# Optimization experiments

Measured on AMD Instinct MI355X. Metric: run time of the kernel, lower is better.

Reference implementation:

```python
import jax, jax.numpy as jnp
import numpy as np

T, B, H = 2048, 64, 256   # time, batch, hidden/input/memory size
A = 256                   # attention_size
IN = H + H                # cell input size = input_size + memory_size = 512
NEG = -1e12


def setup_inputs() -> dict:
    key = jax.random.key(0)
    ks = jax.random.split(key, 12)
    s = lambda k, shape, fan: jax.random.normal(k, shape, jnp.float32) / np.sqrt(fan)
    inp = {
        "input": jax.random.normal(ks[0], (B, H), jnp.float32),
        "memory": jax.random.normal(ks[1], (T, B, H), jnp.float32),
        "memory_mask": jax.random.bernoulli(ks[2], 0.9, (T, B)),
        "state": jax.random.normal(ks[3], (B, H), jnp.float32),
        # attention MLP: Linear(input+state+memory -> A, no bias), Tanh, Linear(A -> 1, no bias)
        "W_a1": s(ks[4], (H + H + H, A), H * 3),
        "w_a2": s(ks[5], (A,), A),
        # gate: Linear(IN -> IN, no bias) + sigmoid
        "W_gate": s(ks[6], (IN, IN), IN),
        # GRUCell params (torch layout: [3H, in], gates order r,z,n)
        "W_ih": s(ks[7], (3 * H, IN), IN),
        "W_hh": s(ks[8], (3 * H, H), H),
        "b_ih": jnp.zeros((3 * H,), jnp.float32),
        "b_hh": jnp.zeros((3 * H,), jnp.float32),
    }
    return inp


def reference(input, memory, memory_mask, state, W_a1, w_a2, W_gate, W_ih, W_hh, b_ih, b_hh):
    # --- additive attention: tanh(W1 @ [input, state, memory]) @ w2 ---
    # split W_a1 by the concat layout [input | state | memory]
    qs = jnp.concatenate([input, state], axis=-1) @ W_a1[: 2 * H]      # [B, A]
    mp = jnp.einsum("tbh,ha->tba", memory, W_a1[2 * H :])               # [T, B, A]
    logits = jnp.tanh(qs[None] + mp) @ w_a2                              # [T, B]
    logits = jnp.where(memory_mask, logits, NEG)
    scores = jax.nn.softmax(logits, axis=0)                              # [T, B]
    attn_vec = jnp.einsum("tb,tbh->bh", scores, memory)                  # [B, H]

    # --- gate ---
    new_input = jnp.concatenate([input, attn_vec], axis=-1)              # [B, 2H]
    gated = new_input * jax.nn.sigmoid(new_input @ W_gate)

    # --- GRU cell (torch semantics, gates r, z, n) ---
    gi = gated @ W_ih.T + b_ih                                           # [B, 3H]
    gh = state @ W_hh.T + b_hh                                           # [B, 3H]
    i_r, i_z, i_n = jnp.split(gi, 3, axis=-1)
    h_r, h_z, h_n = jnp.split(gh, 3, axis=-1)
    r = jax.nn.sigmoid(i_r + h_r)
    z = jax.nn.sigmoid(i_z + h_z)
    n = jnp.tanh(i_n + r * h_n)
    return (1.0 - z) * n + z * state                                     # [B, H]
```

## Files before the change

kernel.cpp:

```cpp
#include <hip/hip_runtime.h>
#include <hip/hip_bf16.h>

#define B_DIM 64
#define H_DIM 256
#define NCHG 8
#define CHUNKS 4
#define TCH 64

typedef __attribute__((ext_vector_type(8))) short short8;
typedef __attribute__((ext_vector_type(4))) float f32x4;

__device__ __forceinline__ unsigned short bfbits(float f) {
    __hip_bfloat16 h = __float2bfloat16(f);
    unsigned short u;
    __builtin_memcpy(&u, &h, 2);
    return u;
}
__device__ __forceinline__ float fexp(float x) {
    float r;
    asm("v_exp_f32 %0, %1" : "=v"(r) : "v"(x * 1.4426950408889634f));
    return r;
}
__device__ __forceinline__ float ftanh(float x) {
    float e, r;
    asm("v_exp_f32 %0, %1" : "=v"(e) : "v"(x * 2.8853900817779268f));
    asm("v_rcp_f32 %0, %1" : "=v"(r) : "v"(e + 1.0f));
    return 1.0f - 2.0f * r;
}
__device__ __forceinline__ float fast_sigmoid(float x) {
    return 1.0f / (1.0f + __expf(-x));
}

__global__ void prep_qs_kernel(const float* __restrict__ W_a1,
                               const float* __restrict__ input,
                               const float* __restrict__ state,
                               unsigned short* __restrict__ WmT,
                               float* __restrict__ qs) {
    __shared__ float cat[512];
    int bid = blockIdx.x, tid = threadIdx.x;
    if (bid < 256) {
        WmT[tid * 256 + bid] = bfbits(W_a1[(512 + bid) * 256 + tid]);
    } else {
        int b = bid - 256;
        cat[tid] = input[b * 256 + tid];
        cat[256 + tid] = state[b * 256 + tid];
        __syncthreads();
        int a = tid;
        float s0 = 0.f, s1 = 0.f, s2 = 0.f, s3 = 0.f;
        #pragma unroll 4
        for (int k = 0; k < 512; k += 4) {
            s0 += cat[k]     * W_a1[(k)     * 256 + a];
            s1 += cat[k + 1] * W_a1[(k + 1) * 256 + a];
            s2 += cat[k + 2] * W_a1[(k + 2) * 256 + a];
            s3 += cat[k + 3] * W_a1[(k + 3) * 256 + a];
        }
        qs[b * 256 + a] = (s0 + s1) + (s2 + s3);
    }
}

__global__ __launch_bounds__(512, 2) void attn_kernel(
    const float* __restrict__ memory, const int* __restrict__ mask,
    const unsigned short* __restrict__ WmT,
    const float* __restrict__ qs, const float* __restrict__ w_a2,
    float* __restrict__ part_l, float* __restrict__ part_acc)
{
    extern __shared__ char smem[];
    unsigned short* slab0 = (unsigned short*)smem;
    unsigned short* slab1 = (unsigned short*)(smem + 32768);
    float* lpart = (float*)(smem + 65536);
    int*   maskL = (int*)(smem + 65536 + 2048);

    int b = blockIdx.x, g = blockIdx.y;
    int tid = threadIdx.x;
    int lane = tid & 63, w = tid >> 6;
    int lr = lane & 15, lh = lane >> 4;
    int tbase = g * (CHUNKS * TCH);
    const float* mbase = memory + (size_t)tbase * (B_DIM * H_DIM) + b * H_DIM;

    float4 ld[8];
    #pragma unroll
    for (int i = 0; i < 8; ++i)
        ld[i] = *((const float4*)(mbase + (size_t)(i * 8 + w) * (B_DIM * H_DIM)) + lane);

    int wa0 = w * 32;
    short8 areg[8][2];
    #pragma unroll
    for (int kk = 0; kk < 8; ++kk)
        #pragma unroll
        for (int mf = 0; mf < 2; ++mf)
            areg[kk][mf] = *(const short8*)(WmT + (wa0 + mf * 16 + lr) * 256 + kk * 32 + lh * 8);

    float qv[2][4], wv[2][4];
    #pragma unroll
    for (int mf = 0; mf < 2; ++mf)
        #pragma unroll
        for (int r = 0; r < 4; ++r) {
            int a = wa0 + mf * 16 + lh * 4 + r;
            qv[mf][r] = qs[b * 256 + a];
            wv[mf][r] = w_a2[a];
        }

    if (tid < CHUNKS * TCH) maskL[tid] = mask[(tbase + tid) * B_DIM + b];

    int wby = (lane * 8) ^ (w << 4);
    #pragma unroll
    for (int i = 0; i < 8; ++i) {
        ushort4 o;
        o.x = bfbits(ld[i].x); o.y = bfbits(ld[i].y);
        o.z = bfbits(ld[i].z); o.w = bfbits(ld[i].w);
        *(ushort4*)((char*)slab0 + (i * 8 + w) * 512 + wby) = o;
    }
    __syncthreads();

    float a8[8] = {0.f, 0.f, 0.f, 0.f, 0.f, 0.f, 0.f, 0.f};
    float l_acc = 0.f;
    int slice4 = ((lane >> 5) + 2 * w) * 4;
    int hpvb = (lane & 31) * 16;

    for (int s = 0; s < CHUNKS; ++s) {
        const char* cur = (const char*)((s & 1) ? slab1 : slab0);
        char* nxt = (char*)((s & 1) ? slab0 : slab1);

        if (s < CHUNKS - 1) {
            #pragma unroll
            for (int i = 0; i < 8; ++i) {
                int row = (s + 1) * TCH + i * 8 + w;
                ld[i] = *((const float4*)(mbase + (size_t)row * (B_DIM * H_DIM)) + lane);
            }
        }

        f32x4 acc[2][4];
        #pragma unroll
        for (int mf = 0; mf < 2; ++mf)
            #pragma unroll
            for (int nf = 0; nf < 4; ++nf)
                acc[mf][nf] = (f32x4){0.f, 0.f, 0.f, 0.f};
        #pragma unroll
        for (int kk = 0; kk < 8; ++kk) {
            int kbyte = kk * 64 + lh * 16;
            #pragma unroll
            for (int nf = 0; nf < 4; ++nf) {
                int t = nf * 16 + lr;
                int sw = kbyte ^ ((t & 7) << 4);
                short8 bfr = *(const short8*)(cur + t * 512 + sw);
                acc[0][nf] = __builtin_amdgcn_mfma_f32_16x16x32_bf16(areg[kk][0], bfr, acc[0][nf], 0, 0, 0);
                acc[1][nf] = __builtin_amdgcn_mfma_f32_16x16x32_bf16(areg[kk][1], bfr, acc[1][nf], 0, 0, 0);
            }
        }

        if (s < CHUNKS - 1) {
            #pragma unroll
            for (int i = 0; i < 8; ++i) {
                ushort4 o;
                o.x = bfbits(ld[i].x); o.y = bfbits(ld[i].y);
                o.z = bfbits(ld[i].z); o.w = bfbits(ld[i].w);
                *(ushort4*)(nxt + (i * 8 + w) * 512 + wby) = o;
            }
        }

        #pragma unroll
        for (int nf = 0; nf < 4; ++nf) {
            float sv = 0.f;
            #pragma unroll
            for (int mf = 0; mf < 2; ++mf)
                #pragma unroll
                for (int r = 0; r < 4; ++r)
                    sv += wv[mf][r] * ftanh(qv[mf][r] + acc[mf][nf][r]);
            sv += __shfl_xor(sv, 16);
            sv += __shfl_xor(sv, 32);
            if (lh == 0) lpart[w * 64 + nf * 16 + lr] = sv;
        }
        __syncthreads();

        float lg = 0.f;
        #pragma unroll
        for (int ww = 0; ww < 8; ++ww) lg += lpart[ww * 64 + lane];
        float pself = maskL[s * 64 + lane] ? fexp(lg) : 0.f;
        if (w == 0) l_acc += pself;

        #pragma unroll
        for (int tt = 0; tt < 4; ++tt) {
            int tl = slice4 + tt;
            float pt = __shfl(pself, tl);
            int swb = hpvb ^ ((tl & 7) << 4);
            uint4 u = *(const uint4*)(cur + tl * 512 + swb);
            a8[0] += pt * __uint_as_float(u.x << 16);
            a8[1] += pt * __uint_as_float(u.x & 0xFFFF0000u);
            a8[2] += pt * __uint_as_float(u.y << 16);
            a8[3] += pt * __uint_as_float(u.y & 0xFFFF0000u);
            a8[4] += pt * __uint_as_float(u.z << 16);
            a8[5] += pt * __uint_as_float(u.z & 0xFFFF0000u);
            a8[6] += pt * __uint_as_float(u.w << 16);
            a8[7] += pt * __uint_as_float(u.w & 0xFFFF0000u);
        }
        __syncthreads();
    }

    float* acc2 = (float*)smem;
    int oct = lane & 31, slice = 2 * w + (lane >> 5), h0 = oct * 8;
    *(float4*)(&acc2[slice * 256 + h0])     = (float4){a8[0], a8[1], a8[2], a8[3]};
    *(float4*)(&acc2[slice * 256 + h0 + 4]) = (float4){a8[4], a8[5], a8[6], a8[7]};
    __syncthreads();
    int pidx = g * B_DIM + b;
    if (tid < 256) {
        float ssum = 0.f;
        #pragma unroll
        for (int sl = 0; sl < 16; ++sl) ssum += acc2[sl * 256 + tid];
        part_acc[(size_t)pidx * 256 + tid] = ssum;
    }
    if (w == 0) {
        #pragma unroll
        for (int d = 1; d < 64; d <<= 1) l_acc += __shfl_xor(l_acc, d);
        if (lane == 0) part_l[pidx] = l_acc;
    }
}

__global__ void mergegate_kernel(const float* __restrict__ part_l,
                                 const float* __restrict__ part_acc,
                                 const float* __restrict__ input,
                                 const float* __restrict__ W_gate,
                                 float* __restrict__ gated) {
    __shared__ float ni[512];
    int b = blockIdx.x, tid = threadIdx.x;
    if (tid >= 256) {
        int k = tid - 256;
        ni[k] = input[b * 256 + k];
    } else {
        int h = tid;
        float L = 0.f, s = 0.f;
        #pragma unroll
        for (int c = 0; c < NCHG; ++c) {
            L += part_l[c * 64 + b];
            s += part_acc[(size_t)(c * 64 + b) * 256 + h];
        }
        ni[256 + h] = s / L;
    }
    __syncthreads();
    int j = tid;
    float s0 = 0.f, s1 = 0.f, s2 = 0.f, s3 = 0.f;
    #pragma unroll 4
    for (int k = 0; k < 512; k += 4) {
        s0 += ni[k]     * W_gate[(k)     * 512 + j];
        s1 += ni[k + 1] * W_gate[(k + 1) * 512 + j];
        s2 += ni[k + 2] * W_gate[(k + 2) * 512 + j];
        s3 += ni[k + 3] * W_gate[(k + 3) * 512 + j];
    }
    float s = (s0 + s1) + (s2 + s3);
    gated[b * 512 + j] = ni[j] * fast_sigmoid(s);
}

__global__ __launch_bounds__(768) void gru_kernel(
    const float* __restrict__ gated, const float* __restrict__ state,
    const float* __restrict__ W_ih, const float* __restrict__ W_hh,
    const float* __restrict__ b_ih, const float* __restrict__ b_hh,
    float* __restrict__ out) {
    __shared__ float ld_g[4][512];
    __shared__ float ld_s[4][256];
    __shared__ float xi[3][16][4];
    __shared__ float xh[3][16][4];
    int ht = blockIdx.x & 15, bt = blockIdx.x >> 4;
    int tid = threadIdx.x;
    #pragma unroll
    for (int i = 0; i < 3; ++i) {
        int idx = i * 768 + tid;
        if (idx < 2048) ld_g[idx >> 9][idx & 511] = gated[(bt * 4 + (idx >> 9)) * 512 + (idx & 511)];
    }
    #pragma unroll
    for (int i = 0; i < 2; ++i) {
        int idx = i * 768 + tid;
        if (idx < 1024) ld_s[idx >> 8][idx & 255] = state[(bt * 4 + (idx >> 8)) * 256 + (idx & 255)];
    }

    int gid = tid >> 4, lk = tid & 15;
    int gate = gid >> 4, hl = gid & 15;
    int j = gate * 256 + ht * 16 + hl;

    float4 wi[8], wh[4];
    #pragma unroll
    for (int it = 0; it < 8; ++it)
        wi[it] = *(const float4*)(W_ih + (size_t)j * 512 + it * 64 + lk * 4);
    #pragma unroll
    for (int it = 0; it < 4; ++it)
        wh[it] = *(const float4*)(W_hh + (size_t)j * 256 + it * 64 + lk * 4);
    float bi = b_ih[j], bh = b_hh[j];
    __syncthreads();

    #pragma unroll
    for (int bb = 0; bb < 4; ++bb) {
        float g0 = 0.f, g1 = 0.f;
        #pragma unroll
        for (int it = 0; it < 8; ++it) {
            float4 gv = *(const float4*)(&ld_g[bb][it * 64 + lk * 4]);
            g0 += wi[it].x * gv.x + wi[it].z * gv.z;
            g1 += wi[it].y * gv.y + wi[it].w * gv.w;
        }
        float h0 = 0.f, h1 = 0.f;
        #pragma unroll
        for (int it = 0; it < 4; ++it) {
            float4 sv = *(const float4*)(&ld_s[bb][it * 64 + lk * 4]);
            h0 += wh[it].x * sv.x + wh[it].z * sv.z;
            h1 += wh[it].y * sv.y + wh[it].w * sv.w;
        }
        float gi_ = g0 + g1, gh_ = h0 + h1;
        #pragma unroll
        for (int m = 1; m < 16; m <<= 1) {
            gi_ += __shfl_xor(gi_, m);
            gh_ += __shfl_xor(gh_, m);
        }
        if (lk == 0) { xi[gate][hl][bb] = gi_ + bi; xh[gate][hl][bb] = gh_ + bh; }
    }
    __syncthreads();
    if (tid < 64) {
        int bb = tid >> 4, hl2 = tid & 15;
        float ir = xi[0][hl2][bb], hr = xh[0][hl2][bb];
        float iz = xi[1][hl2][bb], hz = xh[1][hl2][bb];
        float in_ = xi[2][hl2][bb], hn = xh[2][hl2][bb];
        float r = fast_sigmoid(ir + hr);
        float z = fast_sigmoid(iz + hz);
        float n = 1.0f - 2.0f / (__expf(2.0f * (in_ + r * hn)) + 1.0f);
        out[(bt * 4 + bb) * 256 + ht * 16 + hl2] =
            (1.f - z) * n + z * ld_s[bb][ht * 16 + hl2];
    }
}

extern "C" void kernel_launch(void* const* d_in, const int* in_sizes, int n_in,
                              void* d_out, int out_size, void* d_ws, size_t ws_size,
                              hipStream_t stream) {
    const float* input  = (const float*)d_in[0];
    const float* memory = (const float*)d_in[1];
    const int*   mask   = (const int*)d_in[2];
    const float* state  = (const float*)d_in[3];
    const float* W_a1   = (const float*)d_in[4];
    const float* w_a2   = (const float*)d_in[5];
    const float* W_gate = (const float*)d_in[6];
    const float* W_ih   = (const float*)d_in[7];
    const float* W_hh   = (const float*)d_in[8];
    const float* b_ih   = (const float*)d_in[9];
    const float* b_hh   = (const float*)d_in[10];
    float* out = (float*)d_out;

    char* ws = (char*)d_ws;
    unsigned short* WmT = (unsigned short*)(ws + 0);
    float* qs       = (float*)(ws + 131072);
    float* gated    = (float*)(ws + 196608);
    float* part_l   = (float*)(ws + 327680);
    float* part_acc = (float*)(ws + 335872);

    prep_qs_kernel<<<320, 256, 0, stream>>>(W_a1, input, state, WmT, qs);

    (void)hipFuncSetAttribute((const void*)attn_kernel,
                              hipFuncAttributeMaxDynamicSharedMemorySize, 68608);
    attn_kernel<<<dim3(B_DIM, NCHG), 512, 68608, stream>>>(
        memory, mask, WmT, qs, w_a2, part_l, part_acc);

    mergegate_kernel<<<64, 512, 0, stream>>>(part_l, part_acc, input, W_gate, gated);
    gru_kernel<<<256, 768, 0, stream>>>(gated, state, W_ih, W_hh, b_ih, b_hh, out);
}
```

Before: 79.71 us.

## Deepen attention prefetch to two chunks, halve grid T-split, use lightweight LDS barriers

```diff
diff --git a/kernel.cpp b/kernel.cpp
--- a/kernel.cpp
+++ b/kernel.cpp
@@ -3,8 +3,8 @@
 
 #define B_DIM 64
 #define H_DIM 256
-#define NCHG 8
-#define CHUNKS 4
+#define NCHG 4
+#define CHUNKS 8
 #define TCH 64
 
 typedef __attribute__((ext_vector_type(8))) short short8;
@@ -29,6 +29,11 @@
 }
 __device__ __forceinline__ float fast_sigmoid(float x) {
     return 1.0f / (1.0f + __expf(-x));
+}
+__device__ __forceinline__ void lds_barrier() {
+    asm volatile("s_waitcnt lgkmcnt(0)" ::: "memory");
+    __builtin_amdgcn_s_barrier();
+    __builtin_amdgcn_sched_barrier(0);
 }
 
 __global__ void prep_qs_kernel(const float* __restrict__ W_a1,
@@ -58,7 +63,7 @@
     }
 }
 
-__global__ __launch_bounds__(512, 2) void attn_kernel(
+__global__ __launch_bounds__(512, 1) void attn_kernel(
     const float* __restrict__ memory, const int* __restrict__ mask,
     const unsigned short* __restrict__ WmT,
     const float* __restrict__ qs, const float* __restrict__ w_a2,
@@ -77,11 +82,6 @@
     int tbase = g * (CHUNKS * TCH);
     const float* mbase = memory + (size_t)tbase * (B_DIM * H_DIM) + b * H_DIM;
 
-    float4 ld[8];
-    #pragma unroll
-    for (int i = 0; i < 8; ++i)
-        ld[i] = *((const float4*)(mbase + (size_t)(i * 8 + w) * (B_DIM * H_DIM)) + lane);
-
     int wa0 = w * 32;
     short8 areg[8][2];
     #pragma unroll
@@ -100,33 +100,42 @@
             wv[mf][r] = w_a2[a];
         }
 
-    if (tid < CHUNKS * TCH) maskL[tid] = mask[(tbase + tid) * B_DIM + b];
+    maskL[tid] = mask[(tbase + tid) * B_DIM + b];
 
     int wby = (lane * 8) ^ (w << 4);
-    #pragma unroll
-    for (int i = 0; i < 8; ++i) {
-        ushort4 o;
-        o.x = bfbits(ld[i].x); o.y = bfbits(ld[i].y);
-        o.z = bfbits(ld[i].z); o.w = bfbits(ld[i].w);
-        *(ushort4*)((char*)slab0 + (i * 8 + w) * 512 + wby) = o;
-    }
-    __syncthreads();
+
+    float4 ldA[8], ldB[8];
+#define ISSUE(dst, q)                                                          \
+    _Pragma("unroll") for (int i = 0; i < 8; ++i)                              \
+        dst[i] = *((const float4*)(mbase + (size_t)((q) * TCH + i * 8 + w) *   \
+                                   (B_DIM * H_DIM)) + lane);
+#define WRITE(src, sl)                                                         \
+    _Pragma("unroll") for (int i = 0; i < 8; ++i) {                            \
+        ushort4 o;                                                             \
+        o.x = bfbits(src[i].x); o.y = bfbits(src[i].y);                        \
+        o.z = bfbits(src[i].z); o.w = bfbits(src[i].w);                        \
+        *(ushort4*)((char*)(sl) + (i * 8 + w) * 512 + wby) = o;                \
+    }
+
+    ISSUE(ldA, 0)
+    WRITE(ldA, slab0)
+    ISSUE(ldB, 1)
+    lds_barrier();
 
     float a8[8] = {0.f, 0.f, 0.f, 0.f, 0.f, 0.f, 0.f, 0.f};
     float l_acc = 0.f;
     int slice4 = ((lane >> 5) + 2 * w) * 4;
     int hpvb = (lane & 31) * 16;
 
+    #pragma unroll
     for (int s = 0; s < CHUNKS; ++s) {
-        const char* cur = (const char*)((s & 1) ? slab1 : slab0);
-        char* nxt = (char*)((s & 1) ? slab0 : slab1);
-
-        if (s < CHUNKS - 1) {
-            #pragma unroll
-            for (int i = 0; i < 8; ++i) {
-                int row = (s + 1) * TCH + i * 8 + w;
-                ld[i] = *((const float4*)(mbase + (size_t)row * (B_DIM * H_DIM)) + lane);
-            }
+        char* curp = (char*)((s & 1) ? slab1 : slab0);
+        char* nxtp = (char*)((s & 1) ? slab0 : slab1);
+        const char* cur = curp;
+
+        if (s + 2 < CHUNKS) {
+            if ((s & 1) == 0) { ISSUE(ldA, s + 2) }
+            else              { ISSUE(ldB, s + 2) }
         }
 
         f32x4 acc[2][4];
@@ -148,14 +157,9 @@
             }
         }
 
-        if (s < CHUNKS - 1) {
-            #pragma unroll
-            for (int i = 0; i < 8; ++i) {
-                ushort4 o;
-                o.x = bfbits(ld[i].x); o.y = bfbits(ld[i].y);
-                o.z = bfbits(ld[i].z); o.w = bfbits(ld[i].w);
-                *(ushort4*)(nxt + (i * 8 + w) * 512 + wby) = o;
-            }
+        if (s + 1 < CHUNKS) {
+            if ((s & 1) == 0) { WRITE(ldB, nxtp) }
+            else              { WRITE(ldA, nxtp) }
         }
 
         #pragma unroll
@@ -170,7 +174,7 @@
             sv += __shfl_xor(sv, 32);
             if (lh == 0) lpart[w * 64 + nf * 16 + lr] = sv;
         }
-        __syncthreads();
+        lds_barrier();
 
         float lg = 0.f;
         #pragma unroll
@@ -193,9 +197,12 @@
             a8[6] += pt * __uint_as_float(u.w << 16);
             a8[7] += pt * __uint_as_float(u.w & 0xFFFF0000u);
         }
-        __syncthreads();
-    }
-
+        lds_barrier();
+    }
+#undef ISSUE
+#undef WRITE
+
+    __syncthreads();
     float* acc2 = (float*)smem;
     int oct = lane & 31, slice = 2 * w + (lane >> 5), h0 = oct * 8;
     *(float4*)(&acc2[slice * 256 + h0])     = (float4){a8[0], a8[1], a8[2], a8[3]};
@@ -349,8 +356,8 @@
     prep_qs_kernel<<<320, 256, 0, stream>>>(W_a1, input, state, WmT, qs);
 
     (void)hipFuncSetAttribute((const void*)attn_kernel,
-                              hipFuncAttributeMaxDynamicSharedMemorySize, 68608);
-    attn_kernel<<<dim3(B_DIM, NCHG), 512, 68608, stream>>>(
+                              hipFuncAttributeMaxDynamicSharedMemorySize, 69632);
+    attn_kernel<<<dim3(B_DIM, NCHG), 512, 69632, stream>>>(
         memory, mask, WmT, qs, w_a2, part_l, part_acc);
 
     mergegate_kernel<<<64, 512, 0, stream>>>(part_l, part_acc, input, W_gate, gated);
```

New measurement: 94.22 us. 1.18x slower.
